# Optimization experiments

Hardware: AMD Instinct MI355X
Metric: run time of the kernel (lower is better)

The kernel has to match this reference:

```python
import jax, jax.numpy as jnp
import numpy as np

EPS = 1e-5  # torch LayerNorm default

def _layernorm(x, g, b):
    mu = jnp.mean(x, axis=-1, keepdims=True)
    var = jnp.var(x, axis=-1, keepdims=True)
    return (x - mu) * jax.lax.rsqrt(var + EPS) * g + b

def _mlp(x, g, b, W1, b1, W2, b2):
    # pre-norm LayerNorm -> Linear -> SiLU -> Linear
    h = _layernorm(x, g, b)
    h = jax.nn.silu(h @ W1 + b1)
    return h @ W2 + b2

N, B, F, H = 500_000, 25_000, 128, 64

def setup_inputs() -> dict:
    key = jax.random.key(0)
    ks = jax.random.split(key, 16)
    s = 0.05
    return {
        "pos": jax.random.normal(ks[0], (N, 3), jnp.float32),
        "mass_center": jax.random.normal(ks[1], (B, 3), jnp.float32),
        "scaler": jax.random.normal(ks[2], (N, F), jnp.float32),
        "vector": jax.random.normal(ks[3], (N, 3, F), jnp.float32),
        "batch_index": jnp.sort(jax.random.randint(ks[4], (N,), 0, B)),
        # decoder_alpha params (pre-norm MLP F->H->1)
        "ln_a_g": jnp.ones((F,), jnp.float32),
        "ln_a_b": jnp.zeros((F,), jnp.float32),
        "Wa1": jax.random.normal(ks[5], (F, H), jnp.float32) * s,
        "ba1": jnp.zeros((H,), jnp.float32),
        "Wa2": jax.random.normal(ks[6], (H, 1), jnp.float32) * s,
        "ba2": jnp.zeros((1,), jnp.float32),
        # decoder_nu: gate MLP (pre-norm, F->H->1) + bias-free Linear(F,1)
        "ln_n_g": jnp.ones((F,), jnp.float32),
        "ln_n_b": jnp.zeros((F,), jnp.float32),
        "Wn1": jax.random.normal(ks[7], (F, H), jnp.float32) * s,
        "bn1": jnp.zeros((H,), jnp.float32),
        "Wn2": jax.random.normal(ks[8], (H, 1), jnp.float32) * s,
        "bn2": jnp.zeros((1,), jnp.float32),
        "Wnu": jax.random.normal(ks[9], (F, 1), jnp.float32) * s,
    }

def reference(pos, mass_center, scaler, vector, batch_index,
              ln_a_g, ln_a_b, Wa1, ba1, Wa2, ba2,
              ln_n_g, ln_n_b, Wn1, bn1, Wn2, bn2, Wnu):
    # gather per-node mass center and center positions: [N,3]
    mcv = pos - mass_center[batch_index]
    # Gate: mlp(scaler) [N,1] broadcast-multiplied with vector @ Wnu [N,3,1]
    s_gate = _mlp(scaler, ln_n_g, ln_n_b, Wn1, bn1, Wn2, bn2)       # [N,1]
    v_proj = jnp.einsum('ndf,fo->ndo', vector, Wnu)                  # [N,3,1]
    nu = (s_gate[:, None, :] * v_proj)[..., 0]                       # [N,3]
    # symmetric outer products: [N,3,3]
    outer = nu[:, :, None] * mcv[:, None, :] + mcv[:, :, None] * nu[:, None, :]
    alpha_s = _mlp(scaler, ln_a_g, ln_a_b, Wa1, ba1, Wa2, ba2)       # [N,1]
    alpha = alpha_s[:, :, None] * jnp.eye(3, dtype=alpha_s.dtype) + outer  # [N,3,3]
    # scatter-sum to molecule level, then trace/3
    mol = jax.ops.segment_sum(alpha, batch_index, num_segments=B)    # [B,3,3]
    out = jnp.einsum('bii->b', mol) / 3.0
    return out[:, None]                                              # [B,1]
```

## Files before the change

### kernel.cpp

```cpp
#include <hip/hip_runtime.h>

#define FD 128
#define HD 64
#define NC 128
#define RPB 64

typedef __attribute__((ext_vector_type(8))) short bf16x8;
typedef __attribute__((ext_vector_type(4))) float f32x4;

__device__ __forceinline__ unsigned bfr(float x) {
    unsigned u = __float_as_uint(x);
    return (u + 0x7fffu + ((u >> 16) & 1u)) >> 16;
}

__global__ void prep_kernel(
    const float* __restrict__ lnag, const float* __restrict__ lnab,
    const float* __restrict__ Wa1, const float* __restrict__ ba1, const float* __restrict__ Wa2,
    const float* __restrict__ lnng, const float* __restrict__ lnnb,
    const float* __restrict__ Wn1, const float* __restrict__ bn1, const float* __restrict__ Wn2,
    unsigned short* __restrict__ wq, float* __restrict__ c, float* __restrict__ w2)
{
    int n = threadIdx.x;
    const float* W  = (n < HD) ? Wa1 : Wn1;
    const float* g  = (n < HD) ? lnag : lnng;
    const float* bb = (n < HD) ? lnab : lnnb;
    const float* b1 = (n < HD) ? ba1 : bn1;
    const float* W2 = (n < HD) ? Wa2 : Wn2;
    int h = n & (HD - 1);
    float accb = b1[h];
    for (int f = 0; f < FD; ++f) {
        float w = W[f * HD + h];
        wq[n * FD + f] = (unsigned short)bfr(g[f] * w);
        accb += bb[f] * w;
    }
    c[n] = accb;
    w2[n] = W2[h];
}

__global__ __launch_bounds__(256, 4) void fused_kernel(
    const float* __restrict__ scaler, const float* __restrict__ vec,
    const float* __restrict__ wnu, const float* __restrict__ pos,
    const float* __restrict__ mc, const int* __restrict__ bidx,
    const unsigned short* __restrict__ wq, const float* __restrict__ c,
    const float* __restrict__ w2, const float* __restrict__ ba2,
    const float* __restrict__ bn2, float* __restrict__ out, int n_nodes)
{
    __shared__ uint4 xs[RPB * 16];
    __shared__ float tl[RPB];

    int tid = threadIdx.x;
    int rowbase = blockIdx.x * RPB;
    int lane = tid & 63, w = tid >> 6;

    {
        int o = lane >> 3, cc = lane & 7;
        float4 wn4[4];
#pragma unroll
        for (int m = 0; m < 4; ++m)
            wn4[m] = reinterpret_cast<const float4*>(wnu)[m * 8 + cc];
#pragma unroll
        for (int g = 0; g < 2; ++g) {
            int row = w * 16 + g * 8 + o;
            int node = rowbase + row;
            bool valid = node < n_nodes;
            int n = valid ? node : (n_nodes - 1);
            int b = bidx[n];
            float m0 = pos[n * 3 + 0] - mc[b * 3 + 0];
            float m1 = pos[n * 3 + 1] - mc[b * 3 + 1];
            float m2 = pos[n * 3 + 2] - mc[b * 3 + 2];
            const float4* vr = reinterpret_cast<const float4*>(vec + (size_t)n * 3 * FD);
            float acc = 0.f;
#pragma unroll
            for (int k = 0; k < 12; ++k) {
                float4 v = vr[cc + k * 8];
                float4 wnv = wn4[k & 3];
                float d4 = v.x * wnv.x + v.y * wnv.y + v.z * wnv.z + v.w * wnv.w;
                float mm = (k < 4) ? m0 : (k < 8 ? m1 : m2);
                acc = fmaf(d4, mm, acc);
            }
            acc += __shfl_xor(acc, 1);
            acc += __shfl_xor(acc, 2);
            acc += __shfl_xor(acc, 4);
            if (cc == 0 && valid) tl[row] = acc;
        }
    }

    {
        int r = tid >> 2, qd = tid & 3;
        int node = rowbase + r;
        int gn = node < n_nodes ? node : (n_nodes - 1);
        const float4* rp = reinterpret_cast<const float4*>(scaler + (size_t)gn * FD) + qd * 8;
        float4 v[8];
        float s = 0.f, s2 = 0.f;
#pragma unroll
        for (int i = 0; i < 8; ++i) {
            v[i] = rp[i];
            s  += v[i].x + v[i].y + v[i].z + v[i].w;
            s2 += v[i].x * v[i].x + v[i].y * v[i].y + v[i].z * v[i].z + v[i].w * v[i].w;
        }
        s  += __shfl_xor(s, 1);  s  += __shfl_xor(s, 2);
        s2 += __shfl_xor(s2, 1); s2 += __shfl_xor(s2, 2);
        float mu = s * (1.f / FD);
        float var = s2 * (1.f / FD) - mu * mu;
        float rstd = rsqrtf(var + 1e-5f);
#pragma unroll
        for (int jj = 0; jj < 4; ++jj) {
            float4 a = v[2 * jj], b = v[2 * jj + 1];
            uint4 pk;
            pk.x = bfr((a.x - mu) * rstd) | (bfr((a.y - mu) * rstd) << 16);
            pk.y = bfr((a.z - mu) * rstd) | (bfr((a.w - mu) * rstd) << 16);
            pk.z = bfr((b.x - mu) * rstd) | (bfr((b.y - mu) * rstd) << 16);
            pk.w = bfr((b.z - mu) * rstd) | (bfr((b.w - mu) * rstd) << 16);
            int slot = qd * 4 + jj;
            xs[r * 16 + (slot ^ (r & 15))] = pk;
        }
    }
    __syncthreads();

    int lrow = lane & 15, lgrp = lane >> 4;
    bf16x8 af[4];
#pragma unroll
    for (int ks = 0; ks < 4; ++ks) {
        int r = w * 16 + lrow;
        af[ks] = *reinterpret_cast<const bf16x8*>(&xs[r * 16 + ((ks * 4 + lgrp) ^ (r & 15))]);
    }
    float pa[4] = {0.f, 0.f, 0.f, 0.f}, pn[4] = {0.f, 0.f, 0.f, 0.f};
#pragma unroll
    for (int tile = 0; tile < 8; ++tile) {
        f32x4 acc = {0.f, 0.f, 0.f, 0.f};
        int n = tile * 16 + lrow;
        const bf16x8* brow = reinterpret_cast<const bf16x8*>(wq + n * FD);
#pragma unroll
        for (int ks = 0; ks < 4; ++ks) {
            bf16x8 bf = brow[ks * 4 + lgrp];
            acc = __builtin_amdgcn_mfma_f32_16x16x32_bf16(af[ks], bf, acc, 0, 0, 0);
        }
        int col = tile * 16 + lrow;
        float bias = c[col], w2v = w2[col];
#pragma unroll
        for (int r = 0; r < 4; ++r) {
            float h1 = acc[r] + bias;
            float y = h1 / (1.f + __expf(-h1));
            float cb = y * w2v;
            if (tile < 4) pa[r] += cb; else pn[r] += cb;
        }
    }
#pragma unroll
    for (int off = 1; off < 16; off <<= 1) {
#pragma unroll
        for (int r = 0; r < 4; ++r) {
            pa[r] += __shfl_xor(pa[r], off);
            pn[r] += __shfl_xor(pn[r], off);
        }
    }
    if (lrow == 0) {
        float b2a = ba2[0], b2n = bn2[0];
#pragma unroll
        for (int r = 0; r < 4; ++r) {
            int nl = w * 16 + lgrp * 4 + r;
            int node = rowbase + nl;
            if (node < n_nodes) {
                float val = (pa[r] + b2a) + (2.f / 3.f) * (pn[r] + b2n) * tl[nl];
                atomicAdd(out + bidx[node], val);
            }
        }
    }
}

extern "C" void kernel_launch(void* const* d_in, const int* in_sizes, int n_in,
                              void* d_out, int out_size, void* d_ws, size_t ws_size,
                              hipStream_t stream) {
    const float* pos    = (const float*)d_in[0];
    const float* mc     = (const float*)d_in[1];
    const float* scaler = (const float*)d_in[2];
    const float* vec    = (const float*)d_in[3];
    const int*   bidx   = (const int*)d_in[4];
    const float* lnag   = (const float*)d_in[5];
    const float* lnab   = (const float*)d_in[6];
    const float* Wa1    = (const float*)d_in[7];
    const float* ba1    = (const float*)d_in[8];
    const float* Wa2    = (const float*)d_in[9];
    const float* ba2    = (const float*)d_in[10];
    const float* lnng   = (const float*)d_in[11];
    const float* lnnb   = (const float*)d_in[12];
    const float* Wn1    = (const float*)d_in[13];
    const float* bn1    = (const float*)d_in[14];
    const float* Wn2    = (const float*)d_in[15];
    const float* bn2    = (const float*)d_in[16];
    const float* Wnu    = (const float*)d_in[17];

    int N = in_sizes[0] / 3;
    int B = in_sizes[1] / 3;

    unsigned short* wq = (unsigned short*)d_ws;
    float* c  = (float*)((char*)d_ws + NC * FD * 2);
    float* w2 = c + NC;

    hipMemsetAsync(d_out, 0, (size_t)B * sizeof(float), stream);

    hipLaunchKernelGGL(prep_kernel, dim3(1), dim3(NC), 0, stream,
                       lnag, lnab, Wa1, ba1, Wa2, lnng, lnnb, Wn1, bn1, Wn2, wq, c, w2);

    int blocks = (N + RPB - 1) / RPB;
    hipLaunchKernelGGL(fused_kernel, dim3(blocks), dim3(256), 0, stream,
                       scaler, vec, Wnu, pos, mc, bidx, wq, c, w2, ba2, bn2,
                       (float*)d_out, N);
}
```

Measured before the change: 254.5 us.

## Load scaler rows directly into MFMA A-fragment layout, drop LDS staging and barrier

```diff
diff --git a/kernel.cpp b/kernel.cpp
--- a/kernel.cpp
+++ b/kernel.cpp
@@ -45,12 +45,22 @@
     const float* __restrict__ w2, const float* __restrict__ ba2,
     const float* __restrict__ bn2, float* __restrict__ out, int n_nodes)
 {
-    __shared__ uint4 xs[RPB * 16];
-    __shared__ float tl[RPB];
+    __shared__ float tl[4][16];
 
     int tid = threadIdx.x;
-    int rowbase = blockIdx.x * RPB;
     int lane = tid & 63, w = tid >> 6;
+    int rowbase = blockIdx.x * RPB + w * 16;
+    int lrow = lane & 15, lgrp = lane >> 4;
+
+    int xnode = rowbase + lrow;
+    int gx = xnode < n_nodes ? xnode : (n_nodes - 1);
+    const float4* xp = reinterpret_cast<const float4*>(scaler + (size_t)gx * FD);
+    float4 xv[8];
+#pragma unroll
+    for (int ks = 0; ks < 4; ++ks) {
+        xv[2 * ks]     = xp[ks * 8 + lgrp * 2];
+        xv[2 * ks + 1] = xp[ks * 8 + lgrp * 2 + 1];
+    }
 
     {
         int o = lane >> 3, cc = lane & 7;
@@ -60,10 +70,9 @@
             wn4[m] = reinterpret_cast<const float4*>(wnu)[m * 8 + cc];
 #pragma unroll
         for (int g = 0; g < 2; ++g) {
-            int row = w * 16 + g * 8 + o;
+            int row = g * 8 + o;
             int node = rowbase + row;
-            bool valid = node < n_nodes;
-            int n = valid ? node : (n_nodes - 1);
+            int n = node < n_nodes ? node : (n_nodes - 1);
             int b = bidx[n];
             float m0 = pos[n * 3 + 0] - mc[b * 3 + 0];
             float m1 = pos[n * 3 + 1] - mc[b * 3 + 1];
@@ -81,49 +90,35 @@
             acc += __shfl_xor(acc, 1);
             acc += __shfl_xor(acc, 2);
             acc += __shfl_xor(acc, 4);
-            if (cc == 0 && valid) tl[row] = acc;
-        }
-    }
-
-    {
-        int r = tid >> 2, qd = tid & 3;
-        int node = rowbase + r;
-        int gn = node < n_nodes ? node : (n_nodes - 1);
-        const float4* rp = reinterpret_cast<const float4*>(scaler + (size_t)gn * FD) + qd * 8;
-        float4 v[8];
-        float s = 0.f, s2 = 0.f;
-#pragma unroll
-        for (int i = 0; i < 8; ++i) {
-            v[i] = rp[i];
-            s  += v[i].x + v[i].y + v[i].z + v[i].w;
-            s2 += v[i].x * v[i].x + v[i].y * v[i].y + v[i].z * v[i].z + v[i].w * v[i].w;
-        }
-        s  += __shfl_xor(s, 1);  s  += __shfl_xor(s, 2);
-        s2 += __shfl_xor(s2, 1); s2 += __shfl_xor(s2, 2);
-        float mu = s * (1.f / FD);
-        float var = s2 * (1.f / FD) - mu * mu;
-        float rstd = rsqrtf(var + 1e-5f);
-#pragma unroll
-        for (int jj = 0; jj < 4; ++jj) {
-            float4 a = v[2 * jj], b = v[2 * jj + 1];
-            uint4 pk;
-            pk.x = bfr((a.x - mu) * rstd) | (bfr((a.y - mu) * rstd) << 16);
-            pk.y = bfr((a.z - mu) * rstd) | (bfr((a.w - mu) * rstd) << 16);
-            pk.z = bfr((b.x - mu) * rstd) | (bfr((b.y - mu) * rstd) << 16);
-            pk.w = bfr((b.z - mu) * rstd) | (bfr((b.w - mu) * rstd) << 16);
-            int slot = qd * 4 + jj;
-            xs[r * 16 + (slot ^ (r & 15))] = pk;
-        }
-    }
-    __syncthreads();
-
-    int lrow = lane & 15, lgrp = lane >> 4;
+            if (cc == 0) tl[w][row] = acc;
+        }
+    }
+
+    float s = 0.f, s2 = 0.f;
+#pragma unroll
+    for (int i = 0; i < 8; ++i) {
+        float4 v = xv[i];
+        s  += v.x + v.y + v.z + v.w;
+        s2 += v.x * v.x + v.y * v.y + v.z * v.z + v.w * v.w;
+    }
+    s  += __shfl_xor(s, 16);  s  += __shfl_xor(s, 32);
+    s2 += __shfl_xor(s2, 16); s2 += __shfl_xor(s2, 32);
+    float mu = s * (1.f / FD);
+    float var = s2 * (1.f / FD) - mu * mu;
+    float rstd = rsqrtf(var + 1e-5f);
+
     bf16x8 af[4];
 #pragma unroll
     for (int ks = 0; ks < 4; ++ks) {
-        int r = w * 16 + lrow;
-        af[ks] = *reinterpret_cast<const bf16x8*>(&xs[r * 16 + ((ks * 4 + lgrp) ^ (r & 15))]);
-    }
+        float4 a = xv[2 * ks], b = xv[2 * ks + 1];
+        union { unsigned u[4]; bf16x8 v; } pk;
+        pk.u[0] = bfr((a.x - mu) * rstd) | (bfr((a.y - mu) * rstd) << 16);
+        pk.u[1] = bfr((a.z - mu) * rstd) | (bfr((a.w - mu) * rstd) << 16);
+        pk.u[2] = bfr((b.x - mu) * rstd) | (bfr((b.y - mu) * rstd) << 16);
+        pk.u[3] = bfr((b.z - mu) * rstd) | (bfr((b.w - mu) * rstd) << 16);
+        af[ks] = pk.v;
+    }
+
     float pa[4] = {0.f, 0.f, 0.f, 0.f}, pn[4] = {0.f, 0.f, 0.f, 0.f};
 #pragma unroll
     for (int tile = 0; tile < 8; ++tile) {
@@ -157,10 +152,10 @@
         float b2a = ba2[0], b2n = bn2[0];
 #pragma unroll
         for (int r = 0; r < 4; ++r) {
-            int nl = w * 16 + lgrp * 4 + r;
+            int nl = lgrp * 4 + r;
             int node = rowbase + nl;
             if (node < n_nodes) {
-                float val = (pa[r] + b2a) + (2.f / 3.f) * (pn[r] + b2n) * tl[nl];
+                float val = (pa[r] + b2a) + (2.f / 3.f) * (pn[r] + b2n) * tl[w][nl];
                 atomicAdd(out + bidx[node], val);
             }
         }
```

Result: no change. 251.3 us (-1.2%).
